# Kernel tuning notes

Measured on AMD Instinct MI355X. Metric: run time of the kernel, lower is better.

Reference implementation:

```python
import jax, jax.numpy as jnp
import numpy as np

HEAD_SIZE = 64
NEG_INF = -1.0e9


def setup_inputs() -> dict:
    key = jax.random.key(0)
    ks = jax.random.split(key, 8)
    B, F, T, D, N, H = 4, 2048, 2048, 1024, 16, HEAD_SIZE
    scale = 1.0 / np.sqrt(D)
    return {
        "from_tensor": jax.random.normal(ks[0], (B, F, D), jnp.float32),
        "to_tensor": jax.random.normal(ks[1], (B, T, D), jnp.float32),
        "attention_mask": jax.random.randint(ks[2], (B, T), 0, 2, jnp.int32),
        "wq": jax.random.normal(ks[3], (D, N, H), jnp.float32) * scale,
        "bq": jnp.zeros((N, H), jnp.float32),
        "wk": jax.random.normal(ks[4], (D, N, H), jnp.float32) * scale,
        "bk": jnp.zeros((N, H), jnp.float32),
        "wv": jax.random.normal(ks[5], (D, N, H), jnp.float32) * scale,
        "bv": jnp.zeros((N, H), jnp.float32),
    }


def reference(from_tensor, to_tensor, attention_mask, wq, bq, wk, bk, wv, bv):
    # QKV projections: [B,S,D] x [D,N,H] -> [B,S,N,H]
    q = jnp.einsum("bfd,dnh->bfnh", from_tensor, wq) + bq
    k = jnp.einsum("btd,dnh->btnh", to_tensor, wk) + bk
    v = jnp.einsum("btd,dnh->btnh", to_tensor, wv) + bv
    # scores: [B,N,F,T]
    scores = jnp.einsum("btnh,bfnh->bnft", k, q) * (1.0 / jnp.sqrt(jnp.float32(HEAD_SIZE)))
    # padding mask: positions where attention_mask == 0 get -1e9
    pad = (attention_mask == 0).astype(scores.dtype)[:, None, None, :]
    scores = scores + pad * NEG_INF
    probs = jax.nn.softmax(scores, axis=-1)
    # dropout_rate = 0.0 -> identity
    return jnp.einsum("bnft,btnh->bfnh", probs, v)
```

## Files before the change

### kernel.cpp

```cpp
#include <hip/hip_runtime.h>
#include <hip/hip_bf16.h>
#include <math.h>

typedef __attribute__((ext_vector_type(8))) short bf16x8;
typedef __attribute__((ext_vector_type(4))) float f32x4;

#define SEQ 2048
#define DMODEL 1024
#define NH 16
#define HD 64
#define BATCH 4
#define MROWS (BATCH * SEQ)
#define NOUT (NH * HD)

__device__ inline unsigned bf16pack(float a, float b) {
    unsigned ua = __builtin_bit_cast(unsigned, a);
    unsigned ub = __builtin_bit_cast(unsigned, b);
    ua = (ua + 0x7fffu + ((ua >> 16) & 1u)) >> 16;
    ub = (ub + 0x7fffu + ((ub >> 16) & 1u)) >> 16;
    return ua | (ub << 16);
}

__device__ inline f32x4 f32x4_zero() {
    f32x4 z; z[0] = 0.f; z[1] = 0.f; z[2] = 0.f; z[3] = 0.f; return z;
}

__device__ inline void load_lds16(const void* g, void* l) {
    __builtin_amdgcn_global_load_lds(
        (const __attribute__((address_space(1))) void*)g,
        (__attribute__((address_space(3))) void*)l, 16, 0, 0);
}

__global__ void cast_f32_bf16(const float* __restrict__ in,
                              __hip_bfloat16* __restrict__ out, int n4) {
    int idx = blockIdx.x * 256 + threadIdx.x;
    int stride = gridDim.x * 256;
    for (int i = idx; i < n4; i += stride) {
        float4 v = ((const float4*)in)[i];
        unsigned lo = bf16pack(v.x, v.y), hi = bf16pack(v.z, v.w);
        ((uint2*)out)[i] = make_uint2(lo, hi);
    }
}

__global__ void transpose_cast_w(const float* __restrict__ W,
                                 __hip_bfloat16* __restrict__ Wt) {
    int c0 = blockIdx.x * 16;
    for (int k = threadIdx.x; k < DMODEL; k += 256) {
        #pragma unroll
        for (int c = 0; c < 16; ++c) {
            Wt[(size_t)(c0 + c) * DMODEL + k] =
                __float2bfloat16(W[(size_t)k * NOUT + c0 + c]);
        }
    }
}

template <int TRANS>
__global__ __launch_bounds__(256, 2) void gemm_qkv(
    const __hip_bfloat16* __restrict__ A,
    const __hip_bfloat16* __restrict__ Wt,
    const float* __restrict__ bias,
    __hip_bfloat16* __restrict__ out, float scale) {
    __shared__ __hip_bfloat16 sA[128 * 32];
    __shared__ __hip_bfloat16 sB[128 * 32];
    const int tid = threadIdx.x;
    const int lane = tid & 63, wid = tid >> 6;
    const int wm = wid >> 1, wn = wid & 1;
    const int lrow = lane & 15, lgrp = lane >> 4;
    const int tm = blockIdx.x, tn = blockIdx.y;

    f32x4 acc[4][4];
    #pragma unroll
    for (int i = 0; i < 4; i++)
        #pragma unroll
        for (int j = 0; j < 4; j++) acc[i][j] = f32x4_zero();

    const int idx0 = wid * 64 + lane;

    for (int kt = 0; kt < DMODEL / 32; ++kt) {
        __syncthreads();
        const int k0 = kt * 32;
        #pragma unroll
        for (int c = 0; c < 2; ++c) {
            int idx = c * 256 + idx0;
            int row = idx >> 2, cg = idx & 3;
            const __hip_bfloat16* ga =
                A + ((size_t)tm * 128 + row) * DMODEL + k0 + cg * 8;
            load_lds16(ga, (char*)sA + c * 4096 + wid * 1024);
            const __hip_bfloat16* gb =
                Wt + ((size_t)tn * 128 + row) * DMODEL + k0 + cg * 8;
            load_lds16(gb, (char*)sB + c * 4096 + wid * 1024);
        }
        __syncthreads();

        bf16x8 af[4], bfr[4];
        #pragma unroll
        for (int i = 0; i < 4; i++)
            af[i] = *(const bf16x8*)&sA[(wm * 64 + i * 16 + lrow) * 32 + lgrp * 8];
        #pragma unroll
        for (int j = 0; j < 4; j++)
            bfr[j] = *(const bf16x8*)&sB[(wn * 64 + j * 16 + lrow) * 32 + lgrp * 8];
        #pragma unroll
        for (int i = 0; i < 4; i++)
            #pragma unroll
            for (int j = 0; j < 4; j++)
                acc[i][j] = __builtin_amdgcn_mfma_f32_16x16x32_bf16(
                    af[i], bfr[j], acc[i][j], 0, 0, 0);
    }

    #pragma unroll
    for (int i = 0; i < 4; i++) {
        int mbase = tm * 128 + wm * 64 + i * 16 + lgrp * 4;
        #pragma unroll
        for (int j = 0; j < 4; j++) {
            int cc = tn * 128 + wn * 64 + j * 16 + lrow;
            float bv = bias[cc];
            int n = cc >> 6, h = cc & 63;
            #pragma unroll
            for (int r = 0; r < 4; r++) {
                int mm = mbase + r;
                int b = mm >> 11, s = mm & 2047;
                float val = (acc[i][j][r] + bv) * scale;
                size_t off;
                if (TRANS)
                    off = (((size_t)b * NH + n) * HD + h) * SEQ + s;
                else
                    off = (((size_t)b * NH + n) * SEQ + s) * HD + h;
                out[off] = __float2bfloat16(val);
            }
        }
    }
}

__global__ __launch_bounds__(256, 2) void attn_kernel(
    const __hip_bfloat16* __restrict__ Q,
    const __hip_bfloat16* __restrict__ K,
    const __hip_bfloat16* __restrict__ Vt,
    const int* __restrict__ mask, float* __restrict__ out) {
    __shared__ unsigned short Pt[4][64][68];

    const int tid = threadIdx.x;
    const int lane = tid & 63, wid = tid >> 6;
    const int lrow = lane & 15, lgrp = lane >> 4;
    const int bn = blockIdx.y, b = bn >> 4, n = bn & 15;
    const int qbase = blockIdx.x * 256 + wid * 64;

    const __hip_bfloat16* Qh = Q + (size_t)bn * SEQ * HD;
    const __hip_bfloat16* Kh = K + (size_t)bn * SEQ * HD;
    const __hip_bfloat16* Vh = Vt + (size_t)bn * HD * SEQ;
    const int* mb = mask + b * SEQ;

    bf16x8 qf[4][2];
    #pragma unroll
    for (int i = 0; i < 4; i++)
        #pragma unroll
        for (int k = 0; k < 2; k++)
            qf[i][k] = *(const bf16x8*)(Qh + (size_t)(qbase + i * 16 + lrow) * HD +
                                        k * 32 + lgrp * 8);

    f32x4 o[4][4];
    #pragma unroll
    for (int i = 0; i < 4; i++)
        #pragma unroll
        for (int j = 0; j < 4; j++) o[i][j] = f32x4_zero();
    float lpart[4][4];
    #pragma unroll
    for (int i = 0; i < 4; i++)
        #pragma unroll
        for (int r = 0; r < 4; r++) lpart[i][r] = 0.f;

    for (int tb = 0; tb < SEQ; tb += 64) {
        bf16x8 kf[4][2];
        #pragma unroll
        for (int jc = 0; jc < 4; jc++)
            #pragma unroll
            for (int k = 0; k < 2; k++)
                kf[jc][k] = *(const bf16x8*)(Kh +
                    (size_t)(tb + jc * 16 + lrow) * HD + k * 32 + lgrp * 8);
        bf16x8 vf[4][2];
        #pragma unroll
        for (int jo = 0; jo < 4; jo++)
            #pragma unroll
            for (int tk = 0; tk < 2; tk++)
                vf[jo][tk] = *(const bf16x8*)(Vh +
                    (size_t)(jo * 16 + lrow) * SEQ + tb + tk * 32 + lgrp * 8);

        float madd[4];
        #pragma unroll
        for (int jc = 0; jc < 4; jc++)
            madd[jc] = (mb[tb + jc * 16 + lrow] == 0) ? -1.0e9f : 0.f;

        f32x4 s[4][4];
        #pragma unroll
        for (int i = 0; i < 4; i++)
            #pragma unroll
            for (int jc = 0; jc < 4; jc++) {
                s[i][jc] = __builtin_amdgcn_mfma_f32_16x16x32_bf16(
                    qf[i][0], kf[jc][0], f32x4_zero(), 0, 0, 0);
                s[i][jc] = __builtin_amdgcn_mfma_f32_16x16x32_bf16(
                    qf[i][1], kf[jc][1], s[i][jc], 0, 0, 0);
            }

        #pragma unroll
        for (int i = 0; i < 4; i++)
            #pragma unroll
            for (int jc = 0; jc < 4; jc++) {
                float p0 = exp2f(s[i][jc][0] + madd[jc]);
                float p1 = exp2f(s[i][jc][1] + madd[jc]);
                float p2 = exp2f(s[i][jc][2] + madd[jc]);
                float p3 = exp2f(s[i][jc][3] + madd[jc]);
                lpart[i][0] += p0;
                lpart[i][1] += p1;
                lpart[i][2] += p2;
                lpart[i][3] += p3;
                unsigned u0 = bf16pack(p0, p1);
                unsigned u1 = bf16pack(p2, p3);
                *(uint2*)&Pt[wid][jc * 16 + lrow][i * 16 + lgrp * 4] =
                    make_uint2(u0, u1);
            }

        bf16x8 pa[4][2];
        #pragma unroll
        for (int i = 0; i < 4; i++)
            #pragma unroll
            for (int tk = 0; tk < 2; tk++) {
                bf16x8 v;
                #pragma unroll
                for (int j = 0; j < 8; j++)
                    v[j] = (short)Pt[wid][tk * 32 + lgrp * 8 + j][i * 16 + lrow];
                pa[i][tk] = v;
            }

        #pragma unroll
        for (int i = 0; i < 4; i++)
            #pragma unroll
            for (int jo = 0; jo < 4; jo++) {
                o[i][jo] = __builtin_amdgcn_mfma_f32_16x16x32_bf16(
                    pa[i][0], vf[jo][0], o[i][jo], 0, 0, 0);
                o[i][jo] = __builtin_amdgcn_mfma_f32_16x16x32_bf16(
                    pa[i][1], vf[jo][1], o[i][jo], 0, 0, 0);
            }
    }

    float lst[4][4];
    #pragma unroll
    for (int i = 0; i < 4; i++)
        #pragma unroll
        for (int r = 0; r < 4; r++) {
            float acc = lpart[i][r];
            #pragma unroll
            for (int off = 1; off < 16; off <<= 1)
                acc += __shfl_xor(acc, off, 64);
            lst[i][r] = acc;
        }

    #pragma unroll
    for (int i = 0; i < 4; i++)
        #pragma unroll
        for (int jo = 0; jo < 4; jo++)
            #pragma unroll
            for (int r = 0; r < 4; r++) {
                int q = qbase + i * 16 + lgrp * 4 + r;
                float val = o[i][jo][r] / lst[i][r];
                out[(((size_t)b * SEQ + q) * NH + n) * HD + jo * 16 + lrow] = val;
            }
}

extern "C" void kernel_launch(void* const* d_in, const int* in_sizes, int n_in,
                              void* d_out, int out_size, void* d_ws, size_t ws_size,
                              hipStream_t stream) {
    const float* from = (const float*)d_in[0];
    const float* to   = (const float*)d_in[1];
    const int*  mask  = (const int*)d_in[2];
    const float* wq = (const float*)d_in[3];
    const float* bq = (const float*)d_in[4];
    const float* wk = (const float*)d_in[5];
    const float* bk = (const float*)d_in[6];
    const float* wv = (const float*)d_in[7];
    const float* bv = (const float*)d_in[8];
    float* out = (float*)d_out;

    char* ws = (char*)d_ws;
    const size_t MB = 1024 * 1024;
    __hip_bfloat16* Wtq = (__hip_bfloat16*)(ws + 0 * MB);
    __hip_bfloat16* Wtk = (__hip_bfloat16*)(ws + 2 * MB);
    __hip_bfloat16* Wtv = (__hip_bfloat16*)(ws + 4 * MB);
    __hip_bfloat16* Af  = (__hip_bfloat16*)(ws + 6 * MB);
    __hip_bfloat16* At  = (__hip_bfloat16*)(ws + 22 * MB);
    __hip_bfloat16* Qb  = (__hip_bfloat16*)(ws + 38 * MB);
    __hip_bfloat16* Kb  = (__hip_bfloat16*)(ws + 54 * MB);
    __hip_bfloat16* Vtb = (__hip_bfloat16*)(ws + 70 * MB);

    cast_f32_bf16<<<2048, 256, 0, stream>>>(from, Af, MROWS * DMODEL / 4);
    cast_f32_bf16<<<2048, 256, 0, stream>>>(to, At, MROWS * DMODEL / 4);
    transpose_cast_w<<<64, 256, 0, stream>>>(wq, Wtq);
    transpose_cast_w<<<64, 256, 0, stream>>>(wk, Wtk);
    transpose_cast_w<<<64, 256, 0, stream>>>(wv, Wtv);

    dim3 gg(MROWS / 128, NOUT / 128);
    gemm_qkv<0><<<gg, 256, 0, stream>>>(Af, Wtq, bq, Qb, 0.18033688f);
    gemm_qkv<0><<<gg, 256, 0, stream>>>(At, Wtk, bk, Kb, 1.0f);
    gemm_qkv<1><<<gg, 256, 0, stream>>>(At, Wtv, bv, Vtb, 1.0f);

    dim3 ga(SEQ / 256, BATCH * NH);
    attn_kernel<<<ga, 256, 0, stream>>>(Qb, Kb, Vtb, mask, out);
}
```

Baseline: 413.8 us.

## Merge QKV GEMMs into one launch, remap attention grid, transpose P store

The three projection GEMMs are merged into a single launch, with a sel index on grid y choosing the input, weights, bias, output and transposed layout. This removes two launches and lets the three projections share one grid for better fill. The attention kernel moves to a 1D grid with a swizzled mapping so consecutive workgroups handle different heads, and the P staging buffer is transposed so fragments are read with one 16-byte LDS load instead of eight scalar loads. The cost is four scalar 2-byte LDS stores per tile where there was one 8-byte store, and possible bank conflicts from the new 72-element padding.

```diff
diff --git a/kernel.cpp b/kernel.cpp
--- a/kernel.cpp
+++ b/kernel.cpp
@@ -54,19 +54,33 @@
     }
 }
 
-template <int TRANS>
-__global__ __launch_bounds__(256, 2) void gemm_qkv(
-    const __hip_bfloat16* __restrict__ A,
-    const __hip_bfloat16* __restrict__ Wt,
-    const float* __restrict__ bias,
-    __hip_bfloat16* __restrict__ out, float scale) {
+__global__ __launch_bounds__(256, 2) void gemm_qkv3(
+    const __hip_bfloat16* __restrict__ Af,
+    const __hip_bfloat16* __restrict__ At,
+    const __hip_bfloat16* __restrict__ Wq,
+    const __hip_bfloat16* __restrict__ Wk,
+    const __hip_bfloat16* __restrict__ Wv,
+    const float* __restrict__ bq, const float* __restrict__ bk,
+    const float* __restrict__ bv,
+    __hip_bfloat16* __restrict__ Qb, __hip_bfloat16* __restrict__ Kb,
+    __hip_bfloat16* __restrict__ Vtb, float qscale) {
     __shared__ __hip_bfloat16 sA[128 * 32];
     __shared__ __hip_bfloat16 sB[128 * 32];
     const int tid = threadIdx.x;
     const int lane = tid & 63, wid = tid >> 6;
     const int wm = wid >> 1, wn = wid & 1;
     const int lrow = lane & 15, lgrp = lane >> 4;
-    const int tm = blockIdx.x, tn = blockIdx.y;
+    const int tm = blockIdx.x;
+    const int tny = blockIdx.y;
+    const int sel = tny >> 3;
+    const int tn = tny & 7;
+
+    const __hip_bfloat16* A = sel ? At : Af;
+    const __hip_bfloat16* Wt = (sel == 0) ? Wq : (sel == 1) ? Wk : Wv;
+    const float* bias = (sel == 0) ? bq : (sel == 1) ? bk : bv;
+    __hip_bfloat16* out = (sel == 0) ? Qb : (sel == 1) ? Kb : Vtb;
+    const float scale = sel ? 1.0f : qscale;
+    const bool trans = (sel == 2);
 
     f32x4 acc[4][4];
     #pragma unroll
@@ -113,15 +127,15 @@
         #pragma unroll
         for (int j = 0; j < 4; j++) {
             int cc = tn * 128 + wn * 64 + j * 16 + lrow;
-            float bv = bias[cc];
+            float bv_ = bias[cc];
             int n = cc >> 6, h = cc & 63;
             #pragma unroll
             for (int r = 0; r < 4; r++) {
                 int mm = mbase + r;
                 int b = mm >> 11, s = mm & 2047;
-                float val = (acc[i][j][r] + bv) * scale;
+                float val = (acc[i][j][r] + bv_) * scale;
                 size_t off;
-                if (TRANS)
+                if (trans)
                     off = (((size_t)b * NH + n) * HD + h) * SEQ + s;
                 else
                     off = (((size_t)b * NH + n) * SEQ + s) * HD + h;
@@ -136,13 +150,18 @@
     const __hip_bfloat16* __restrict__ K,
     const __hip_bfloat16* __restrict__ Vt,
     const int* __restrict__ mask, float* __restrict__ out) {
-    __shared__ unsigned short Pt[4][64][68];
+    __shared__ unsigned short Ptq[4][64][72];
 
     const int tid = threadIdx.x;
     const int lane = tid & 63, wid = tid >> 6;
     const int lrow = lane & 15, lgrp = lane >> 4;
-    const int bn = blockIdx.y, b = bn >> 4, n = bn & 15;
-    const int qbase = blockIdx.x * 256 + wid * 64;
+
+    const int wg = blockIdx.x;
+    const int work = ((wg & 7) << 6) | (wg >> 3);
+    const int bn = work >> 3;
+    const int qblk = work & 7;
+    const int b = bn >> 4, n = bn & 15;
+    const int qbase = qblk * 256 + wid * 64;
 
     const __hip_bfloat16* Qh = Q + (size_t)bn * SEQ * HD;
     const __hip_bfloat16* Kh = K + (size_t)bn * SEQ * HD;
@@ -214,21 +233,21 @@
                 lpart[i][3] += p3;
                 unsigned u0 = bf16pack(p0, p1);
                 unsigned u1 = bf16pack(p2, p3);
-                *(uint2*)&Pt[wid][jc * 16 + lrow][i * 16 + lgrp * 4] =
-                    make_uint2(u0, u1);
+                const int qb = i * 16 + lgrp * 4;
+                const int tt = jc * 16 + lrow;
+                Ptq[wid][qb + 0][tt] = (unsigned short)u0;
+                Ptq[wid][qb + 1][tt] = (unsigned short)(u0 >> 16);
+                Ptq[wid][qb + 2][tt] = (unsigned short)u1;
+                Ptq[wid][qb + 3][tt] = (unsigned short)(u1 >> 16);
             }
 
         bf16x8 pa[4][2];
         #pragma unroll
         for (int i = 0; i < 4; i++)
             #pragma unroll
-            for (int tk = 0; tk < 2; tk++) {
-                bf16x8 v;
-                #pragma unroll
-                for (int j = 0; j < 8; j++)
-                    v[j] = (short)Pt[wid][tk * 32 + lgrp * 8 + j][i * 16 + lrow];
-                pa[i][tk] = v;
-            }
+            for (int tk = 0; tk < 2; tk++)
+                pa[i][tk] = *(const bf16x8*)
+                    &Ptq[wid][i * 16 + lrow][tk * 32 + lgrp * 8];
 
         #pragma unroll
         for (int i = 0; i < 4; i++)
@@ -296,11 +315,8 @@
     transpose_cast_w<<<64, 256, 0, stream>>>(wk, Wtk);
     transpose_cast_w<<<64, 256, 0, stream>>>(wv, Wtv);
 
-    dim3 gg(MROWS / 128, NOUT / 128);
-    gemm_qkv<0><<<gg, 256, 0, stream>>>(Af, Wtq, bq, Qb, 0.18033688f);
-    gemm_qkv<0><<<gg, 256, 0, stream>>>(At, Wtk, bk, Kb, 1.0f);
-    gemm_qkv<1><<<gg, 256, 0, stream>>>(At, Wtv, bv, Vtb, 1.0f);
-
-    dim3 ga(SEQ / 256, BATCH * NH);
-    attn_kernel<<<ga, 256, 0, stream>>>(Qb, Kb, Vtb, mask, out);
-}
+    gemm_qkv3<<<dim3(MROWS / 128, 24), 256, 0, stream>>>(
+        Af, At, Wtq, Wtk, Wtv, bq, bk, bv, Qb, Kb, Vtb, 0.18033688f);
+
+    attn_kernel<<<512, 256, 0, stream>>>(Qb, Kb, Vtb, mask, out);
+}
```

New measurement: 382.1 us. 7.7% less time.
